# Optimization experiments

Measured on AMD Instinct MI355X. Metric: run time of the kernel, lower is better.

Reference implementation:

```python
import jax, jax.numpy as jnp
import numpy as np

B, L = 128, 256
VOCAB, E, PF = 50000, 300, 50
C, K, R = 512, 3, 53
D3 = (E + 2 * PF) * 3  # 1200, conv input channels


def setup_inputs() -> dict:
    key = jax.random.key(0)
    ks = jax.random.split(key, 12)
    return {
        "context": jax.random.randint(ks[0], (B, L), 0, VOCAB),
        "subject_idx": jnp.sort(jax.random.randint(ks[1], (B, 2), 0, L), axis=-1),
        "object_idx": jnp.sort(jax.random.randint(ks[2], (B, 2), 0, L), axis=-1),
        "subject_dis": jax.random.randint(ks[3], (B, L), 0, 2 * L),
        "object_dis": jax.random.randint(ks[4], (B, L), 0, 2 * L),
        "embed_table": jax.random.normal(ks[5], (VOCAB, E), dtype=jnp.float32),
        "pos_table": jax.random.normal(ks[6], (2 * L, PF), dtype=jnp.float32),
        "conv_w": jax.random.normal(ks[7], (C, D3, K), dtype=jnp.float32) * (1.0 / np.sqrt(D3 * K)),
        "conv_b": jax.random.normal(ks[8], (C,), dtype=jnp.float32) * 0.01,
        "rela_linear_w": jax.random.normal(ks[9], (R, C), dtype=jnp.float32) * (1.0 / np.sqrt(C)),
        "rela_emb": jax.random.normal(ks[10], (R, C), dtype=jnp.float32),
    }


def _span_mean(wf3, idx):
    # mean of wf3[b, start:end+1, :] per sample, vectorized with a mask
    pos = jnp.arange(wf3.shape[1])[None, :]
    m = ((pos >= idx[:, 0:1]) & (pos <= idx[:, 1:2])).astype(wf3.dtype)  # B,L
    return jnp.einsum("bld,bl->bd", wf3, m) / jnp.sum(m, axis=1, keepdims=True)


def reference(context, subject_idx, object_idx, subject_dis, object_dis,
              embed_table, pos_table, conv_w, conv_b, rela_linear_w, rela_emb):
    emb = embed_table[context]                                            # B,L,E
    posf = jnp.concatenate([pos_table[subject_dis], pos_table[object_dis]], axis=2)
    wf = jnp.concatenate([emb, posf], axis=2)                             # B,L,D
    wp = jnp.pad(wf, ((0, 0), (1, 1), (0, 0)))
    # sliding window concat of [i-1, i, i+1]
    wf3 = jnp.concatenate([wp[:, :-2], wp[:, 1:-1], wp[:, 2:]], axis=2)   # B,L,3D

    subj = _span_mean(wf3, subject_idx)                                   # B,3D
    obj = _span_mean(wf3, object_idx)
    rs = jax.nn.softmax(jnp.einsum("bld,bd->bl", wf3, subj), axis=1)
    ro = jax.nn.softmax(jnp.einsum("bld,bd->bl", wf3, obj), axis=1)
    wf3 = wf3 * ((rs + ro) * 0.5)[:, :, None]

    x = jnp.transpose(wf3, (0, 2, 1))                                     # B,3D,L
    y = jax.lax.conv_general_dilated(x, conv_w, (1,), [(K // 2, K // 2)],
                                     dimension_numbers=("NCH", "OIH", "NCH"))
    sent = jnp.transpose(jnp.tanh(y + conv_b[None, :, None]), (0, 2, 1))  # B,L,C

    attn = jnp.einsum("blr,rc->blc",
                      jnp.einsum("blc,rc->blr", sent, rela_linear_w), rela_emb)
    attn = jax.nn.softmax(attn, axis=1)  # softmax over sequence positions
    wo = jnp.max(sent * attn, axis=1)                                     # B,C
    wo = wo / jnp.maximum(jnp.linalg.norm(wo, axis=1, keepdims=True), 1e-12)
    all_dist = jnp.linalg.norm(wo[:, None, :] - rela_emb[None, :, :], axis=2)  # B,R
    return all_dist
```

## Files before the change

### kernel.cpp

```cpp
#include <hip/hip_runtime.h>
#include <hip/hip_bf16.h>
#include <math.h>

#define B_  128
#define L_  256
#define E_  300
#define PF_ 50
#define D_  400
#define D3_ 1200
#define C_  512
#define KW_ 3
#define R_  53
#define M_  (B_*L_)
#define KP_ 1216
#define K3_ (3*KP_)
#define LROWS_ 258

typedef __attribute__((ext_vector_type(8))) short bf16x8;
typedef __attribute__((ext_vector_type(8))) unsigned short u16x8;
typedef __attribute__((ext_vector_type(4))) float f32x4;

__device__ __forceinline__ unsigned short f2bf(float f) {
    union { float f; unsigned u; } x; x.f = f;
    unsigned r = x.u + 0x7FFF + ((x.u >> 16) & 1);
    return (unsigned short)(r >> 16);
}
__device__ __forceinline__ float bf2f(unsigned short u) {
    union { unsigned u; float f; } x; x.u = ((unsigned)u) << 16;
    return x.f;
}

__device__ __forceinline__ void gld16(const void* g, void* l) {
    __builtin_amdgcn_global_load_lds(
        (const __attribute__((address_space(1))) void*)g,
        (__attribute__((address_space(3))) void*)l, 16, 0, 0);
}

__global__ void prep_wpT_kernel(const float* __restrict__ conv_w, unsigned short* __restrict__ WpT) {
    int idx = blockIdx.x * blockDim.x + threadIdx.x;
    if (idx >= C_ * K3_) return;
    int c = idx / K3_, q = idx % K3_;
    int k = q / KP_, ch = q % KP_;
    WpT[idx] = (ch < D3_) ? f2bf(conv_w[c * (D3_ * KW_) + ch * KW_ + k]) : (unsigned short)0;
}

__global__ void prep_mT_kernel(const float* __restrict__ rlw, const float* __restrict__ re,
                               unsigned short* __restrict__ MmatT) {
    int idx = blockIdx.x * blockDim.x + threadIdx.x;
    if (idx >= C_ * C_) return;
    int n = idx / C_, k = idx % C_;
    float acc = 0.f;
    for (int r = 0; r < R_; ++r)
        acc += rlw[r * C_ + k] * re[r * C_ + n];
    MmatT[idx] = f2bf(acc);
}

__global__ void build_wf_kernel(const int* __restrict__ ctx, const int* __restrict__ sdis,
                                const int* __restrict__ odis, const float* __restrict__ emb,
                                const float* __restrict__ pos, float* __restrict__ wf) {
    const int total = M_ * D_;
    for (int idx = blockIdx.x * blockDim.x + threadIdx.x; idx < total;
         idx += gridDim.x * blockDim.x) {
        int d = idx % D_;
        int bt = idx / D_;
        float v;
        if (d < E_)            v = emb[(long)ctx[bt] * E_ + d];
        else if (d < E_ + PF_) v = pos[sdis[bt] * PF_ + (d - E_)];
        else                   v = pos[odis[bt] * PF_ + (d - E_ - PF_)];
        wf[idx] = v;
    }
}

__global__ __launch_bounds__(512) void span_sum_kernel(
    const float* __restrict__ wf, const int* __restrict__ sidx, const int* __restrict__ oidx,
    float* __restrict__ SS, float* __restrict__ OS) {
    const int b = blockIdx.x, e = blockIdx.y;
    const int* idx = e ? oidx : sidx;
    float* out = e ? OS : SS;
    const int s0 = idx[b * 2], s1 = idx[b * 2 + 1];
    const float inv = 1.f / (float)(s1 - s0 + 1);
    const int d = threadIdx.x;
    if (d >= D_) return;

    const float* base_p = wf + (size_t)(b << 8) * D_ + d;
    float base = 0.f;
    for (int t = s0; t <= s1; ++t) base += base_p[(size_t)t * D_];

    float w_s0 = base_p[(size_t)s0 * D_];
    float w_s1 = base_p[(size_t)s1 * D_];
    float j0 = base - w_s1 + ((s0 > 0) ? base_p[(size_t)(s0 - 1) * D_] : 0.f);
    float j2 = base - w_s0 + ((s1 < L_ - 1) ? base_p[(size_t)(s1 + 1) * D_] : 0.f);

    out[((size_t)(b * 3 + 0)) * D_ + d] = j0 * inv;
    out[((size_t)(b * 3 + 1)) * D_ + d] = base * inv;
    out[((size_t)(b * 3 + 2)) * D_ + d] = j2 * inv;
}

__global__ __launch_bounds__(256) void dots_kernel(
    const float* __restrict__ wf, const float* __restrict__ SS, const float* __restrict__ OS,
    float* __restrict__ dsb, float* __restrict__ ddb) {
    const int wave = threadIdx.x >> 6, lane = threadIdx.x & 63;
    const int g = blockIdx.x * 4 + wave;
    const int b = g >> 8, t = g & 255;
    float ds = 0.f, dd = 0.f;
#pragma unroll
    for (int j = 0; j < 3; ++j) {
        int u = t + j - 1;
        if ((unsigned)u < (unsigned)L_) {
            const float4* w  = (const float4*)(wf + ((size_t)((b << 8) + u)) * D_);
            const float4* ss = (const float4*)(SS + ((size_t)(b * 3 + j)) * D_);
            const float4* oo = (const float4*)(OS + ((size_t)(b * 3 + j)) * D_);
            for (int q = lane; q < D_ / 4; q += 64) {
                float4 wv = w[q], sv = ss[q], ov = oo[q];
                ds += wv.x * sv.x + wv.y * sv.y + wv.z * sv.z + wv.w * sv.w;
                dd += wv.x * ov.x + wv.y * ov.y + wv.z * ov.z + wv.w * ov.w;
            }
        }
    }
#pragma unroll
    for (int off = 32; off > 0; off >>= 1) {
        ds += __shfl_down(ds, off);
        dd += __shfl_down(dd, off);
    }
    if (lane == 0) { dsb[g] = ds; ddb[g] = dd; }
}

__global__ __launch_bounds__(256) void softmax_s_kernel(
    const float* __restrict__ dsb, const float* __restrict__ ddb, float* __restrict__ s) {
    const int b = blockIdx.x, tid = threadIdx.x;
    __shared__ float red[256];
    float ds = dsb[(b << 8) + tid];
    float dd = ddb[(b << 8) + tid];

    red[tid] = ds; __syncthreads();
    for (int st = 128; st > 0; st >>= 1) {
        if (tid < st) red[tid] = fmaxf(red[tid], red[tid + st]);
        __syncthreads();
    }
    float ms = red[0]; __syncthreads();
    float es = expf(ds - ms);
    red[tid] = es; __syncthreads();
    for (int st = 128; st > 0; st >>= 1) {
        if (tid < st) red[tid] += red[tid + st];
        __syncthreads();
    }
    float zs = red[0]; __syncthreads();

    red[tid] = dd; __syncthreads();
    for (int st = 128; st > 0; st >>= 1) {
        if (tid < st) red[tid] = fmaxf(red[tid], red[tid + st]);
        __syncthreads();
    }
    float mo = red[0]; __syncthreads();
    float eo = expf(dd - mo);
    red[tid] = eo; __syncthreads();
    for (int st = 128; st > 0; st >>= 1) {
        if (tid < st) red[tid] += red[tid + st];
        __syncthreads();
    }
    float zo = red[0];

    s[(b << 8) + tid] = 0.5f * (es / zs + eo / zo);
}

__global__ void build_xsp_kernel(const float* __restrict__ wf, const float* __restrict__ s,
                                 unsigned short* __restrict__ XSp) {
    const int CH8 = KP_ / 8;
    int idx = blockIdx.x * blockDim.x + threadIdx.x;
    const int total = B_ * LROWS_ * CH8;
    if (idx >= total) return;
    int chunk = idx % CH8;
    int rb = idx / CH8;
    int row = rb % LROWS_;
    int b = rb / LROWS_;

    u16x8 out = {0,0,0,0,0,0,0,0};
    int t = row - 1;
    int ch0 = chunk * 8;
    if ((unsigned)t < (unsigned)L_ && ch0 < D3_) {
        int j = ch0 / D_;
        int d0 = ch0 - j * D_;
        int u = t + j - 1;
        if ((unsigned)u < (unsigned)L_) {
            float sc = s[(b << 8) + t];
            const float* w = wf + ((size_t)((b << 8) + u)) * D_ + d0;
#pragma unroll
            for (int q = 0; q < 8; ++q) out[q] = f2bf(sc * w[q]);
        }
    }
    *(u16x8*)&XSp[((size_t)(b * LROWS_ + row)) * KP_ + ch0] = out;
}

template<int MODE>
__global__ __launch_bounds__(512, 2) void gemm8_kernel(
    const unsigned short* __restrict__ Aglob, const unsigned short* __restrict__ Bglob,
    const float* __restrict__ conv_b, unsigned short* __restrict__ outb,
    float* __restrict__ outf) {
    extern __shared__ unsigned short lds[];
    const int tid = threadIdx.x;
    const int lane = tid & 63;
    const int wave = tid >> 6;
    const int wr = wave >> 2;
    const int wc = wave & 3;
    const int bx = blockIdx.x;
    const int blockN = blockIdx.y * 256;
    const int l15 = lane & 15;
    const int NT = (MODE == 0) ? (K3_ / 64) : (C_ / 64);
    const size_t Astr = (MODE == 0) ? (size_t)KP_ : (size_t)C_;
    const size_t Bstr = (MODE == 0) ? (size_t)K3_ : (size_t)C_;

    const int arole = wc;
    const int bhalf = wc >> 1;
    const int brole = wr * 2 + (wc & 1);

    const int acol0 = (((lane >> 4) + 0) ^ (l15 & 7)) * 8;
    const int acol1 = (((lane >> 4) + 4) ^ (l15 & 7)) * 8;
    const int bro = (wc & 1) * 64;

    auto stageA = [&](int kt, int buf) {
        const unsigned short* gb;
        if constexpr (MODE == 0) {
            int tap = kt / KP_, ch0 = kt - tap * KP_;
            gb = Aglob + ((size_t)(bx * LROWS_ + wr * 128 + tap)) * KP_ + ch0;
        } else {
            gb = Aglob + ((size_t)(bx * 256 + wr * 128)) * C_ + kt;
        }
        unsigned short* pb = &lds[(buf * 2 + wr) * 8192];
#pragma unroll
        for (int i = 0; i < 4; ++i) {
            int sl = arole * 256 + i * 64 + lane;
            int row = sl >> 3, p = sl & 7;
            int colg = p ^ (row & 7);
            gld16(gb + (size_t)row * Astr + colg * 8, (char*)pb + sl * 16);
        }
    };
    auto stageB = [&](int kt, int buf) {
        const unsigned short* gb = Bglob + ((size_t)(blockN + bhalf * 128)) * Bstr + kt;
        unsigned short* pb = &lds[32768 + (buf * 2 + bhalf) * 8192];
#pragma unroll
        for (int i = 0; i < 4; ++i) {
            int sl = brole * 256 + i * 64 + lane;
            int row = sl >> 3, p = sl & 7;
            int colg = p ^ (row & 7);
            gld16(gb + (size_t)row * Bstr + colg * 8, (char*)pb + sl * 16);
        }
    };

    f32x4 acc[8][4] = {};

    stageA(0, 0);
    stageB(0, 0);
    __syncthreads();

    int cur = 0;
    for (int kt = 0; kt < NT * 64; kt += 64, cur ^= 1) {
        int ktn = kt + 64;
        if (ktn >= NT * 64) ktn = 0;
        const unsigned short* Ap = &lds[(cur * 2 + wr) * 8192];
        const unsigned short* Bp = &lds[32768 + (cur * 2 + bhalf) * 8192];

        bf16x8 a[8], b0, b1;

#pragma unroll
        for (int mi = 0; mi < 8; ++mi) a[mi] = *(const bf16x8*)&Ap[(mi * 16 + l15) * 64 + acol0];
        b0 = *(const bf16x8*)&Bp[(bro + 0 * 16 + l15) * 64 + acol0];
        b1 = *(const bf16x8*)&Bp[(bro + 1 * 16 + l15) * 64 + acol0];
        stageA(ktn, cur ^ 1);
        __builtin_amdgcn_s_setprio(1);
#pragma unroll
        for (int mi = 0; mi < 8; ++mi) {
            acc[mi][0] = __builtin_amdgcn_mfma_f32_16x16x32_bf16(a[mi], b0, acc[mi][0], 0, 0, 0);
            acc[mi][1] = __builtin_amdgcn_mfma_f32_16x16x32_bf16(a[mi], b1, acc[mi][1], 0, 0, 0);
        }
        __builtin_amdgcn_s_setprio(0);

        b0 = *(const bf16x8*)&Bp[(bro + 2 * 16 + l15) * 64 + acol0];
        b1 = *(const bf16x8*)&Bp[(bro + 3 * 16 + l15) * 64 + acol0];
        stageB(ktn, cur ^ 1);
        __builtin_amdgcn_s_setprio(1);
#pragma unroll
        for (int mi = 0; mi < 8; ++mi) {
            acc[mi][2] = __builtin_amdgcn_mfma_f32_16x16x32_bf16(a[mi], b0, acc[mi][2], 0, 0, 0);
            acc[mi][3] = __builtin_amdgcn_mfma_f32_16x16x32_bf16(a[mi], b1, acc[mi][3], 0, 0, 0);
        }
        __builtin_amdgcn_s_setprio(0);

#pragma unroll
        for (int mi = 0; mi < 8; ++mi) a[mi] = *(const bf16x8*)&Ap[(mi * 16 + l15) * 64 + acol1];
        b0 = *(const bf16x8*)&Bp[(bro + 0 * 16 + l15) * 64 + acol1];
        b1 = *(const bf16x8*)&Bp[(bro + 1 * 16 + l15) * 64 + acol1];
        __builtin_amdgcn_s_setprio(1);
#pragma unroll
        for (int mi = 0; mi < 8; ++mi) {
            acc[mi][0] = __builtin_amdgcn_mfma_f32_16x16x32_bf16(a[mi], b0, acc[mi][0], 0, 0, 0);
            acc[mi][1] = __builtin_amdgcn_mfma_f32_16x16x32_bf16(a[mi], b1, acc[mi][1], 0, 0, 0);
        }
        __builtin_amdgcn_s_setprio(0);

        b0 = *(const bf16x8*)&Bp[(bro + 2 * 16 + l15) * 64 + acol1];
        b1 = *(const bf16x8*)&Bp[(bro + 3 * 16 + l15) * 64 + acol1];
        __builtin_amdgcn_s_setprio(1);
#pragma unroll
        for (int mi = 0; mi < 8; ++mi) {
            acc[mi][2] = __builtin_amdgcn_mfma_f32_16x16x32_bf16(a[mi], b0, acc[mi][2], 0, 0, 0);
            acc[mi][3] = __builtin_amdgcn_mfma_f32_16x16x32_bf16(a[mi], b1, acc[mi][3], 0, 0, 0);
        }
        __builtin_amdgcn_s_setprio(0);

        __syncthreads();
    }

    const int r4 = ((lane >> 4) << 2);
#pragma unroll
    for (int mi = 0; mi < 8; ++mi) {
#pragma unroll
        for (int nj = 0; nj < 4; ++nj) {
            const int col = blockN + wc * 64 + nj * 16 + l15;
            const int row0 = bx * 256 + wr * 128 + mi * 16 + r4;
            if constexpr (MODE == 0) {
                float bias = conv_b[col];
#pragma unroll
                for (int r = 0; r < 4; ++r)
                    outb[(size_t)(row0 + r) * C_ + col] = f2bf(tanhf(acc[mi][nj][r] + bias));
            } else {
#pragma unroll
                for (int r = 0; r < 4; ++r)
                    outf[(size_t)(row0 + r) * C_ + col] = acc[mi][nj][r];
            }
        }
    }
}

__global__ __launch_bounds__(256) void softmax_wo_kernel(
    const float* __restrict__ P, const unsigned short* __restrict__ sent,
    float* __restrict__ wo) {
    const int b = blockIdx.x;
    const int c = blockIdx.y * 256 + threadIdx.x;
    const float* Pb = P + ((size_t)(b << 8)) * C_ + c;
    const unsigned short* Sb = sent + ((size_t)(b << 8)) * C_ + c;
    float m = -INFINITY;
    for (int l = 0; l < L_; ++l) m = fmaxf(m, Pb[(size_t)l * C_]);
    float z = 0.f, wmax = -INFINITY;
    for (int l = 0; l < L_; ++l) {
        float e = expf(Pb[(size_t)l * C_] - m);
        z += e;
        wmax = fmaxf(wmax, bf2f(Sb[(size_t)l * C_]) * e);
    }
    wo[b * C_ + c] = wmax / z;
}

__global__ __launch_bounds__(256) void final_kernel(
    const float* __restrict__ wo, const float* __restrict__ re, float* __restrict__ out) {
    const int b = blockIdx.x, tid = threadIdx.x;
    __shared__ float won[C_];
    __shared__ float red[256];
    float p = 0.f;
    for (int c = tid; c < C_; c += 256) {
        float v = wo[b * C_ + c];
        p += v * v;
    }
    red[tid] = p; __syncthreads();
    for (int st = 128; st > 0; st >>= 1) {
        if (tid < st) red[tid] += red[tid + st];
        __syncthreads();
    }
    float inv = 1.f / fmaxf(sqrtf(red[0]), 1e-12f);
    for (int c = tid; c < C_; c += 256) won[c] = wo[b * C_ + c] * inv;
    __syncthreads();
    const int wv = tid >> 6, lane = tid & 63;
    for (int r = wv; r < R_; r += 4) {
        float acc2 = 0.f;
        for (int c = lane; c < C_; c += 64) {
            float dlt = won[c] - re[r * C_ + c];
            acc2 += dlt * dlt;
        }
        for (int off = 32; off > 0; off >>= 1) acc2 += __shfl_down(acc2, off);
        if (lane == 0) out[b * R_ + r] = sqrtf(acc2);
    }
}

extern "C" void kernel_launch(void* const* d_in, const int* in_sizes, int n_in,
                              void* d_out, int out_size, void* d_ws, size_t ws_size,
                              hipStream_t stream) {
    const int* context     = (const int*)d_in[0];
    const int* subject_idx = (const int*)d_in[1];
    const int* object_idx  = (const int*)d_in[2];
    const int* subject_dis = (const int*)d_in[3];
    const int* object_dis  = (const int*)d_in[4];
    const float* embed_table = (const float*)d_in[5];
    const float* pos_table   = (const float*)d_in[6];
    const float* conv_w      = (const float*)d_in[7];
    const float* conv_b      = (const float*)d_in[8];
    const float* rlw         = (const float*)d_in[9];
    const float* re          = (const float*)d_in[10];
    float* out = (float*)d_out;

    char* ws = (char*)d_ws;
    size_t off = 0;
    auto alloc = [&](size_t bytes) {
        void* p = ws + off;
        off = (off + bytes + 255) & ~(size_t)255;
        return p;
    };
    float* wf            = (float*)alloc((size_t)M_ * D_ * 4);
    float* s             = (float*)alloc((size_t)M_ * 4);
    unsigned short* XSp  = (unsigned short*)alloc((size_t)B_ * LROWS_ * KP_ * 2);
    unsigned short* WpT  = (unsigned short*)alloc((size_t)C_ * K3_ * 2);
    unsigned short* MmatT= (unsigned short*)alloc((size_t)C_ * C_ * 2);
    unsigned short* sent = (unsigned short*)alloc((size_t)M_ * C_ * 2);
    float* wo            = (float*)alloc((size_t)B_ * C_ * 4);
    float* SS            = (float*)alloc((size_t)B_ * 3 * D_ * 4);
    float* OS            = (float*)alloc((size_t)B_ * 3 * D_ * 4);
    float* dsb           = (float*)alloc((size_t)M_ * 4);
    float* ddb           = (float*)alloc((size_t)M_ * 4);
    float* P = (float*)XSp;

    (void)hipFuncSetAttribute((const void*)gemm8_kernel<0>,
                              hipFuncAttributeMaxDynamicSharedMemorySize, 131072);
    (void)hipFuncSetAttribute((const void*)gemm8_kernel<1>,
                              hipFuncAttributeMaxDynamicSharedMemorySize, 131072);

    prep_wpT_kernel<<<(C_ * K3_ + 255) / 256, 256, 0, stream>>>(conv_w, WpT);
    prep_mT_kernel<<<(C_ * C_ + 255) / 256, 256, 0, stream>>>(rlw, re, MmatT);
    build_wf_kernel<<<4096, 256, 0, stream>>>(context, subject_dis, object_dis,
                                              embed_table, pos_table, wf);
    span_sum_kernel<<<dim3(B_, 2), 512, 0, stream>>>(wf, subject_idx, object_idx, SS, OS);
    dots_kernel<<<M_ / 4, 256, 0, stream>>>(wf, SS, OS, dsb, ddb);
    softmax_s_kernel<<<B_, 256, 0, stream>>>(dsb, ddb, s);
    build_xsp_kernel<<<(B_ * LROWS_ * (KP_ / 8) + 255) / 256, 256, 0, stream>>>(wf, s, XSp);
    gemm8_kernel<0><<<dim3(M_ / 256, C_ / 256), 512, 131072, stream>>>(
        XSp, WpT, conv_b, sent, nullptr);
    gemm8_kernel<1><<<dim3(M_ / 256, C_ / 256), 512, 131072, stream>>>(
        sent, MmatT, nullptr, nullptr, P);
    softmax_wo_kernel<<<dim3(B_, 2), 256, 0, stream>>>(P, sent, wo);
    final_kernel<<<B_, 256, 0, stream>>>(wo, re, out);
}
```

Baseline: 345.6 us.

## Split conv GEMM into quadrant-staged pipeline with interleaved half-tile loads

Replaces the templated conv GEMM with a dedicated kernel that splits the 256x256 block tile into four 128x128 quadrants. Each half-tile of A and B is staged into LDS separately and interleaved with the MFMA work on other quadrants, using explicit vmcnt waits and barriers. This aims to overlap global-to-LDS loads with compute at a finer grain and to shorten the stall before each k-step. The second GEMM becomes a plain specialized kernel with the same logic as before. The hand-tuned waitcnt accounting carries a correctness risk if the outstanding-load counts are wrong.

```diff
diff --git a/kernel.cpp b/kernel.cpp
--- a/kernel.cpp
+++ b/kernel.cpp
@@ -191,11 +191,173 @@
     *(u16x8*)&XSp[((size_t)(b * LROWS_ + row)) * KP_ + ch0] = out;
 }
 
-template<int MODE>
-__global__ __launch_bounds__(512, 2) void gemm8_kernel(
-    const unsigned short* __restrict__ Aglob, const unsigned short* __restrict__ Bglob,
-    const float* __restrict__ conv_b, unsigned short* __restrict__ outb,
-    float* __restrict__ outf) {
+__global__ __launch_bounds__(512, 2) void conv_m201_kernel(
+    const unsigned short* __restrict__ XSp, const unsigned short* __restrict__ WpT,
+    const float* __restrict__ conv_b, unsigned short* __restrict__ sent) {
+    extern __shared__ unsigned short lds[];
+    const int tid = threadIdx.x;
+    const int lane = tid & 63;
+    const int wave = tid >> 6;
+    const int wr2 = wave >> 2;
+    const int wc2 = wave & 3;
+    const int bx = blockIdx.x;
+    const int blockN = blockIdx.y * 256;
+    const int l15 = lane & 15;
+    const int rg = lane >> 4;
+    const int sw = l15 & 7;
+    const int NT = K3_ / 64;
+    const int colk0 = ((0 * 4 + rg) ^ sw) * 8;
+    const int colk1 = ((1 * 4 + rg) ^ sw) * 8;
+
+    auto stageA = [&](int kt, int d, int h) {
+        int tap = kt / KP_, ch0 = kt - tap * KP_;
+        const unsigned short* ga = XSp + ((size_t)(bx * LROWS_ + h * 128 + tap)) * KP_ + ch0;
+        unsigned short* pb = &lds[(d * 2 + h) * 8192];
+#pragma unroll
+        for (int i = 0; i < 2; ++i) {
+            int sl = i * 512 + tid;
+            int row = sl >> 3, p = sl & 7;
+            int colg = p ^ (row & 7);
+            gld16(ga + (size_t)row * KP_ + colg * 8, (char*)pb + sl * 16);
+        }
+    };
+    auto stageB = [&](int kt, int d, int h) {
+        const unsigned short* gb = WpT + ((size_t)(blockN + h * 128)) * K3_ + kt;
+        unsigned short* pb = &lds[32768 + (d * 2 + h) * 8192];
+#pragma unroll
+        for (int i = 0; i < 2; ++i) {
+            int sl = i * 512 + tid;
+            int row = sl >> 3, p = sl & 7;
+            int colg = p ^ (row & 7);
+            gld16(gb + (size_t)row * K3_ + colg * 8, (char*)pb + sl * 16);
+        }
+    };
+
+    f32x4 acc[4][4][2] = {};
+
+    stageA(0, 0, 0); stageB(0, 0, 0); stageA(0, 0, 1); stageB(0, 0, 1);
+    stageA(64 < NT * 64 ? 64 : 0, 1, 0); stageB(64 < NT * 64 ? 64 : 0, 1, 0);
+    asm volatile("s_waitcnt vmcnt(4)" ::: "memory");
+    __builtin_amdgcn_s_barrier();
+
+    int d = 0;
+    for (int t = 0; t < NT; ++t, d ^= 1) {
+        const int t1 = (t + 1 < NT) ? t + 1 : 0;
+        const int t2 = (t + 2 < NT) ? t + 2 : t + 2 - NT;
+        const int kt1 = t1 * 64, kt2 = t2 * 64;
+        const unsigned short* A0 = &lds[(d * 2 + 0) * 8192];
+        const unsigned short* A1 = &lds[(d * 2 + 1) * 8192];
+        const unsigned short* B0 = &lds[32768 + (d * 2 + 0) * 8192];
+        const unsigned short* B1 = &lds[32768 + (d * 2 + 1) * 8192];
+
+        bf16x8 a[4][2], bh0[2][2], bh1[2][2];
+
+#pragma unroll
+        for (int mi = 0; mi < 4; ++mi) {
+            int row = wr2 * 64 + mi * 16 + l15;
+            a[mi][0] = *(const bf16x8*)&A0[row * 64 + colk0];
+            a[mi][1] = *(const bf16x8*)&A0[row * 64 + colk1];
+        }
+#pragma unroll
+        for (int ni = 0; ni < 2; ++ni) {
+            int row = wc2 * 32 + ni * 16 + l15;
+            bh0[ni][0] = *(const bf16x8*)&B0[row * 64 + colk0];
+            bh0[ni][1] = *(const bf16x8*)&B0[row * 64 + colk1];
+        }
+        stageB(kt1, d ^ 1, 1);
+        __builtin_amdgcn_s_barrier();
+        __builtin_amdgcn_s_setprio(1);
+#pragma unroll
+        for (int mi = 0; mi < 4; ++mi)
+#pragma unroll
+            for (int ni = 0; ni < 2; ++ni)
+#pragma unroll
+                for (int ks = 0; ks < 2; ++ks)
+                    acc[0][mi][ni] = __builtin_amdgcn_mfma_f32_16x16x32_bf16(
+                        a[mi][ks], bh0[ni][ks], acc[0][mi][ni], 0, 0, 0);
+        __builtin_amdgcn_s_setprio(0);
+        __builtin_amdgcn_s_barrier();
+
+#pragma unroll
+        for (int ni = 0; ni < 2; ++ni) {
+            int row = wc2 * 32 + ni * 16 + l15;
+            bh1[ni][0] = *(const bf16x8*)&B1[row * 64 + colk0];
+            bh1[ni][1] = *(const bf16x8*)&B1[row * 64 + colk1];
+        }
+        stageA(kt1, d ^ 1, 1);
+        asm volatile("s_waitcnt vmcnt(6)" ::: "memory");
+        __builtin_amdgcn_s_barrier();
+        __builtin_amdgcn_s_setprio(1);
+#pragma unroll
+        for (int mi = 0; mi < 4; ++mi)
+#pragma unroll
+            for (int ni = 0; ni < 2; ++ni)
+#pragma unroll
+                for (int ks = 0; ks < 2; ++ks)
+                    acc[1][mi][ni] = __builtin_amdgcn_mfma_f32_16x16x32_bf16(
+                        a[mi][ks], bh1[ni][ks], acc[1][mi][ni], 0, 0, 0);
+        __builtin_amdgcn_s_setprio(0);
+        __builtin_amdgcn_s_barrier();
+
+#pragma unroll
+        for (int mi = 0; mi < 4; ++mi) {
+            int row = wr2 * 64 + mi * 16 + l15;
+            a[mi][0] = *(const bf16x8*)&A1[row * 64 + colk0];
+            a[mi][1] = *(const bf16x8*)&A1[row * 64 + colk1];
+        }
+        stageA(kt2, d, 0);
+        __builtin_amdgcn_s_barrier();
+        __builtin_amdgcn_s_setprio(1);
+#pragma unroll
+        for (int mi = 0; mi < 4; ++mi)
+#pragma unroll
+            for (int ni = 0; ni < 2; ++ni)
+#pragma unroll
+                for (int ks = 0; ks < 2; ++ks)
+                    acc[2][mi][ni] = __builtin_amdgcn_mfma_f32_16x16x32_bf16(
+                        a[mi][ks], bh0[ni][ks], acc[2][mi][ni], 0, 0, 0);
+        __builtin_amdgcn_s_setprio(0);
+        __builtin_amdgcn_s_barrier();
+
+        stageB(kt2, d, 0);
+        asm volatile("s_waitcnt vmcnt(6)" ::: "memory");
+        __builtin_amdgcn_s_barrier();
+        __builtin_amdgcn_s_setprio(1);
+#pragma unroll
+        for (int mi = 0; mi < 4; ++mi)
+#pragma unroll
+            for (int ni = 0; ni < 2; ++ni)
+#pragma unroll
+                for (int ks = 0; ks < 2; ++ks)
+                    acc[3][mi][ni] = __builtin_amdgcn_mfma_f32_16x16x32_bf16(
+                        a[mi][ks], bh1[ni][ks], acc[3][mi][ni], 0, 0, 0);
+        __builtin_amdgcn_s_setprio(0);
+        __builtin_amdgcn_s_barrier();
+    }
+
+    asm volatile("s_waitcnt vmcnt(0)" ::: "memory");
+
+    const int r4 = (lane >> 4) << 2;
+#pragma unroll
+    for (int q = 0; q < 4; ++q) {
+#pragma unroll
+        for (int mi = 0; mi < 4; ++mi) {
+#pragma unroll
+            for (int ni = 0; ni < 2; ++ni) {
+                const int col = blockN + (q & 1) * 128 + wc2 * 32 + ni * 16 + l15;
+                const int row0 = bx * 256 + (q >> 1) * 128 + wr2 * 64 + mi * 16 + r4;
+                float bias = conv_b[col];
+#pragma unroll
+                for (int r = 0; r < 4; ++r)
+                    sent[(size_t)(row0 + r) * C_ + col] = f2bf(tanhf(acc[q][mi][ni][r] + bias));
+            }
+        }
+    }
+}
+
+__global__ __launch_bounds__(512, 2) void pgemm_kernel(
+    const unsigned short* __restrict__ sent, const unsigned short* __restrict__ MmatT,
+    float* __restrict__ P) {
     extern __shared__ unsigned short lds[];
     const int tid = threadIdx.x;
     const int lane = tid & 63;
@@ -205,9 +367,7 @@
     const int bx = blockIdx.x;
     const int blockN = blockIdx.y * 256;
     const int l15 = lane & 15;
-    const int NT = (MODE == 0) ? (K3_ / 64) : (C_ / 64);
-    const size_t Astr = (MODE == 0) ? (size_t)KP_ : (size_t)C_;
-    const size_t Bstr = (MODE == 0) ? (size_t)K3_ : (size_t)C_;
+    const int NT = C_ / 64;
 
     const int arole = wc;
     const int bhalf = wc >> 1;
@@ -218,31 +378,25 @@
     const int bro = (wc & 1) * 64;
 
     auto stageA = [&](int kt, int buf) {
-        const unsigned short* gb;
-        if constexpr (MODE == 0) {
-            int tap = kt / KP_, ch0 = kt - tap * KP_;
-            gb = Aglob + ((size_t)(bx * LROWS_ + wr * 128 + tap)) * KP_ + ch0;
-        } else {
-            gb = Aglob + ((size_t)(bx * 256 + wr * 128)) * C_ + kt;
-        }
+        const unsigned short* gb = sent + ((size_t)(bx * 256 + wr * 128)) * C_ + kt;
         unsigned short* pb = &lds[(buf * 2 + wr) * 8192];
 #pragma unroll
         for (int i = 0; i < 4; ++i) {
             int sl = arole * 256 + i * 64 + lane;
             int row = sl >> 3, p = sl & 7;
             int colg = p ^ (row & 7);
-            gld16(gb + (size_t)row * Astr + colg * 8, (char*)pb + sl * 16);
+            gld16(gb + (size_t)row * C_ + colg * 8, (char*)pb + sl * 16);
         }
     };
     auto stageB = [&](int kt, int buf) {
-        const unsigned short* gb = Bglob + ((size_t)(blockN + bhalf * 128)) * Bstr + kt;
+        const unsigned short* gb = MmatT + ((size_t)(blockN + bhalf * 128)) * C_ + kt;
         unsigned short* pb = &lds[32768 + (buf * 2 + bhalf) * 8192];
 #pragma unroll
         for (int i = 0; i < 4; ++i) {
             int sl = brole * 256 + i * 64 + lane;
             int row = sl >> 3, p = sl & 7;
             int colg = p ^ (row & 7);
-            gld16(gb + (size_t)row * Bstr + colg * 8, (char*)pb + sl * 16);
+            gld16(gb + (size_t)row * C_ + colg * 8, (char*)pb + sl * 16);
         }
     };
 
@@ -317,16 +471,9 @@
         for (int nj = 0; nj < 4; ++nj) {
             const int col = blockN + wc * 64 + nj * 16 + l15;
             const int row0 = bx * 256 + wr * 128 + mi * 16 + r4;
-            if constexpr (MODE == 0) {
-                float bias = conv_b[col];
-#pragma unroll
-                for (int r = 0; r < 4; ++r)
-                    outb[(size_t)(row0 + r) * C_ + col] = f2bf(tanhf(acc[mi][nj][r] + bias));
-            } else {
-#pragma unroll
-                for (int r = 0; r < 4; ++r)
-                    outf[(size_t)(row0 + r) * C_ + col] = acc[mi][nj][r];
-            }
+#pragma unroll
+            for (int r = 0; r < 4; ++r)
+                P[(size_t)(row0 + r) * C_ + col] = acc[mi][nj][r];
         }
     }
 }
@@ -415,9 +562,9 @@
     float* ddb           = (float*)alloc((size_t)M_ * 4);
     float* P = (float*)XSp;
 
-    (void)hipFuncSetAttribute((const void*)gemm8_kernel<0>,
+    (void)hipFuncSetAttribute((const void*)conv_m201_kernel,
                               hipFuncAttributeMaxDynamicSharedMemorySize, 131072);
-    (void)hipFuncSetAttribute((const void*)gemm8_kernel<1>,
+    (void)hipFuncSetAttribute((const void*)pgemm_kernel,
                               hipFuncAttributeMaxDynamicSharedMemorySize, 131072);
 
     prep_wpT_kernel<<<(C_ * K3_ + 255) / 256, 256, 0, stream>>>(conv_w, WpT);
@@ -428,10 +575,9 @@
     dots_kernel<<<M_ / 4, 256, 0, stream>>>(wf, SS, OS, dsb, ddb);
     softmax_s_kernel<<<B_, 256, 0, stream>>>(dsb, ddb, s);
     build_xsp_kernel<<<(B_ * LROWS_ * (KP_ / 8) + 255) / 256, 256, 0, stream>>>(wf, s, XSp);
-    gemm8_kernel<0><<<dim3(M_ / 256, C_ / 256), 512, 131072, stream>>>(
-        XSp, WpT, conv_b, sent, nullptr);
-    gemm8_kernel<1><<<dim3(M_ / 256, C_ / 256), 512, 131072, stream>>>(
-        sent, MmatT, nullptr, nullptr, P);
+    conv_m201_kernel<<<dim3(M_ / 256, C_ / 256), 512, 131072, stream>>>(
+        XSp, WpT, conv_b, sent);
+    pgemm_kernel<<<dim3(M_ / 256, C_ / 256), 512, 131072, stream>>>(sent, MmatT, P);
     softmax_wo_kernel<<<dim3(B_, 2), 256, 0, stream>>>(P, sent, wo);
     final_kernel<<<B_, 256, 0, stream>>>(wo, re, out);
 }
```

Result: slower. 356.1 us (+3.0%).

## Split conv GEMM into dedicated kernel with triple-buffered 32-wide K pipeline

Applied to the files above, without the earlier changes.

The conv GEMM gets its own kernel. It uses a K tile of 32 instead of 64 and triple-buffered LDS with two tiles in flight, waiting on a partial vmcnt before each barrier so loads overlap the MFMAs. The LDS swizzle changes to a rotation pattern suited to 32-element rows, and dynamic LDS drops to 96KB. This should hide more global load latency, at the cost of twice as many barriers and loop iterations per K. The second GEMM is moved unchanged into a specialised non-templated kernel.

```diff
diff --git a/kernel.cpp b/kernel.cpp
--- a/kernel.cpp
+++ b/kernel.cpp
@@ -191,11 +191,9 @@
     *(u16x8*)&XSp[((size_t)(b * LROWS_ + row)) * KP_ + ch0] = out;
 }
 
-template<int MODE>
-__global__ __launch_bounds__(512, 2) void gemm8_kernel(
-    const unsigned short* __restrict__ Aglob, const unsigned short* __restrict__ Bglob,
-    const float* __restrict__ conv_b, unsigned short* __restrict__ outb,
-    float* __restrict__ outf) {
+__global__ __launch_bounds__(512, 2) void conv32_kernel(
+    const unsigned short* __restrict__ XSp, const unsigned short* __restrict__ WpT,
+    const float* __restrict__ conv_b, unsigned short* __restrict__ sent) {
     extern __shared__ unsigned short lds[];
     const int tid = threadIdx.x;
     const int lane = tid & 63;
@@ -205,44 +203,140 @@
     const int bx = blockIdx.x;
     const int blockN = blockIdx.y * 256;
     const int l15 = lane & 15;
-    const int NT = (MODE == 0) ? (K3_ / 64) : (C_ / 64);
-    const size_t Astr = (MODE == 0) ? (size_t)KP_ : (size_t)C_;
-    const size_t Bstr = (MODE == 0) ? (size_t)K3_ : (size_t)C_;
-
+    const int NT = K3_ / 32;
     const int arole = wc;
     const int bhalf = wc >> 1;
     const int brole = wr * 2 + (wc & 1);
+    const int bro = (wc & 1) * 64;
+    const int acolp = (((lane >> 4) + (l15 >> 1)) & 3) * 8;
+
+    auto stageA = [&](int kt, int buf) {
+        int tap = kt / KP_, ch0 = kt - tap * KP_;
+        const unsigned short* ga = XSp + ((size_t)(bx * LROWS_ + wr * 128 + tap)) * KP_ + ch0;
+        unsigned short* pb = &lds[(buf * 2 + wr) * 4096];
+#pragma unroll
+        for (int i = 0; i < 2; ++i) {
+            int sl = arole * 128 + i * 64 + lane;
+            int row = sl >> 2, p = sl & 3;
+            int g = (p - (row >> 1)) & 3;
+            gld16(ga + (size_t)row * KP_ + g * 8, (char*)pb + sl * 16);
+        }
+    };
+    auto stageB = [&](int kt, int buf) {
+        const unsigned short* gb = WpT + ((size_t)(blockN + bhalf * 128)) * K3_ + kt;
+        unsigned short* pb = &lds[16384 + (buf * 2 + bhalf) * 4096];
+#pragma unroll
+        for (int i = 0; i < 2; ++i) {
+            int sl = brole * 128 + i * 64 + lane;
+            int row = sl >> 2, p = sl & 3;
+            int g = (p - (row >> 1)) & 3;
+            gld16(gb + (size_t)row * K3_ + g * 8, (char*)pb + sl * 16);
+        }
+    };
+
+    f32x4 acc[8][4] = {};
+
+    stageA(0, 0); stageB(0, 0);
+    stageA(32, 1); stageB(32, 1);
+    asm volatile("s_waitcnt vmcnt(4)" ::: "memory");
+    __builtin_amdgcn_s_barrier();
+    asm volatile("" ::: "memory");
+
+    int cur = 0, tgt = 2;
+    for (int t = 0; t < NT; ++t) {
+        int t2 = t + 2;
+        if (t2 >= NT) t2 -= NT;
+        const int kt2 = t2 * 32;
+        const unsigned short* Ap = &lds[(cur * 2 + wr) * 4096];
+        const unsigned short* Bp = &lds[16384 + (cur * 2 + bhalf) * 4096];
+
+        bf16x8 a[8], b[4];
+#pragma unroll
+        for (int mi = 0; mi < 8; ++mi)
+            a[mi] = *(const bf16x8*)&Ap[(mi * 16 + l15) * 32 + acolp];
+#pragma unroll
+        for (int ni = 0; ni < 4; ++ni)
+            b[ni] = *(const bf16x8*)&Bp[(bro + ni * 16 + l15) * 32 + acolp];
+
+        stageA(kt2, tgt);
+        stageB(kt2, tgt);
+
+        __builtin_amdgcn_s_setprio(1);
+#pragma unroll
+        for (int mi = 0; mi < 8; ++mi)
+#pragma unroll
+            for (int ni = 0; ni < 4; ++ni)
+                acc[mi][ni] = __builtin_amdgcn_mfma_f32_16x16x32_bf16(
+                    a[mi], b[ni], acc[mi][ni], 0, 0, 0);
+        __builtin_amdgcn_s_setprio(0);
+
+        asm volatile("s_waitcnt vmcnt(4)" ::: "memory");
+        __builtin_amdgcn_s_barrier();
+        asm volatile("" ::: "memory");
+
+        cur = (cur == 2) ? 0 : cur + 1;
+        tgt = (tgt == 2) ? 0 : tgt + 1;
+    }
+
+    asm volatile("s_waitcnt vmcnt(0)" ::: "memory");
+
+    const int r4 = ((lane >> 4) << 2);
+#pragma unroll
+    for (int mi = 0; mi < 8; ++mi) {
+#pragma unroll
+        for (int nj = 0; nj < 4; ++nj) {
+            const int col = blockN + wc * 64 + nj * 16 + l15;
+            const int row0 = bx * 256 + wr * 128 + mi * 16 + r4;
+            float bias = conv_b[col];
+#pragma unroll
+            for (int r = 0; r < 4; ++r)
+                sent[(size_t)(row0 + r) * C_ + col] = f2bf(tanhf(acc[mi][nj][r] + bias));
+        }
+    }
+}
+
+__global__ __launch_bounds__(512, 2) void pgemm_kernel(
+    const unsigned short* __restrict__ sent, const unsigned short* __restrict__ MmatT,
+    float* __restrict__ P) {
+    extern __shared__ unsigned short lds[];
+    const int tid = threadIdx.x;
+    const int lane = tid & 63;
+    const int wave = tid >> 6;
+    const int wr = wave >> 2;
+    const int wc = wave & 3;
+    const int bx = blockIdx.x;
+    const int blockN = blockIdx.y * 256;
+    const int l15 = lane & 15;
+    const int NT = C_ / 64;
+
+    const int arole = wc;
+    const int bhalf = wc >> 1;
+    const int brole = wr * 2 + (wc & 1);
 
     const int acol0 = (((lane >> 4) + 0) ^ (l15 & 7)) * 8;
     const int acol1 = (((lane >> 4) + 4) ^ (l15 & 7)) * 8;
     const int bro = (wc & 1) * 64;
 
     auto stageA = [&](int kt, int buf) {
-        const unsigned short* gb;
-        if constexpr (MODE == 0) {
-            int tap = kt / KP_, ch0 = kt - tap * KP_;
-            gb = Aglob + ((size_t)(bx * LROWS_ + wr * 128 + tap)) * KP_ + ch0;
-        } else {
-            gb = Aglob + ((size_t)(bx * 256 + wr * 128)) * C_ + kt;
-        }
+        const unsigned short* gb = sent + ((size_t)(bx * 256 + wr * 128)) * C_ + kt;
         unsigned short* pb = &lds[(buf * 2 + wr) * 8192];
 #pragma unroll
         for (int i = 0; i < 4; ++i) {
             int sl = arole * 256 + i * 64 + lane;
             int row = sl >> 3, p = sl & 7;
             int colg = p ^ (row & 7);
-            gld16(gb + (size_t)row * Astr + colg * 8, (char*)pb + sl * 16);
+            gld16(gb + (size_t)row * C_ + colg * 8, (char*)pb + sl * 16);
         }
     };
     auto stageB = [&](int kt, int buf) {
-        const unsigned short* gb = Bglob + ((size_t)(blockN + bhalf * 128)) * Bstr + kt;
+        const unsigned short* gb = MmatT + ((size_t)(blockN + bhalf * 128)) * C_ + kt;
         unsigned short* pb = &lds[32768 + (buf * 2 + bhalf) * 8192];
 #pragma unroll
         for (int i = 0; i < 4; ++i) {
             int sl = brole * 256 + i * 64 + lane;
             int row = sl >> 3, p = sl & 7;
             int colg = p ^ (row & 7);
-            gld16(gb + (size_t)row * Bstr + colg * 8, (char*)pb + sl * 16);
+            gld16(gb + (size_t)row * C_ + colg * 8, (char*)pb + sl * 16);
         }
     };
 
@@ -317,16 +411,9 @@
         for (int nj = 0; nj < 4; ++nj) {
             const int col = blockN + wc * 64 + nj * 16 + l15;
             const int row0 = bx * 256 + wr * 128 + mi * 16 + r4;
-            if constexpr (MODE == 0) {
-                float bias = conv_b[col];
-#pragma unroll
-                for (int r = 0; r < 4; ++r)
-                    outb[(size_t)(row0 + r) * C_ + col] = f2bf(tanhf(acc[mi][nj][r] + bias));
-            } else {
-#pragma unroll
-                for (int r = 0; r < 4; ++r)
-                    outf[(size_t)(row0 + r) * C_ + col] = acc[mi][nj][r];
-            }
+#pragma unroll
+            for (int r = 0; r < 4; ++r)
+                P[(size_t)(row0 + r) * C_ + col] = acc[mi][nj][r];
         }
     }
 }
@@ -415,9 +502,9 @@
     float* ddb           = (float*)alloc((size_t)M_ * 4);
     float* P = (float*)XSp;
 
-    (void)hipFuncSetAttribute((const void*)gemm8_kernel<0>,
-                              hipFuncAttributeMaxDynamicSharedMemorySize, 131072);
-    (void)hipFuncSetAttribute((const void*)gemm8_kernel<1>,
+    (void)hipFuncSetAttribute((const void*)conv32_kernel,
+                              hipFuncAttributeMaxDynamicSharedMemorySize, 98304);
+    (void)hipFuncSetAttribute((const void*)pgemm_kernel,
                               hipFuncAttributeMaxDynamicSharedMemorySize, 131072);
 
     prep_wpT_kernel<<<(C_ * K3_ + 255) / 256, 256, 0, stream>>>(conv_w, WpT);
@@ -428,10 +515,9 @@
     dots_kernel<<<M_ / 4, 256, 0, stream>>>(wf, SS, OS, dsb, ddb);
     softmax_s_kernel<<<B_, 256, 0, stream>>>(dsb, ddb, s);
     build_xsp_kernel<<<(B_ * LROWS_ * (KP_ / 8) + 255) / 256, 256, 0, stream>>>(wf, s, XSp);
-    gemm8_kernel<0><<<dim3(M_ / 256, C_ / 256), 512, 131072, stream>>>(
-        XSp, WpT, conv_b, sent, nullptr);
-    gemm8_kernel<1><<<dim3(M_ / 256, C_ / 256), 512, 131072, stream>>>(
-        sent, MmatT, nullptr, nullptr, P);
+    conv32_kernel<<<dim3(M_ / 256, C_ / 256), 512, 98304, stream>>>(
+        XSp, WpT, conv_b, sent);
+    pgemm_kernel<<<dim3(M_ / 256, C_ / 256), 512, 131072, stream>>>(sent, MmatT, P);
     softmax_wo_kernel<<<dim3(B_, 2), 256, 0, stream>>>(P, sent, wo);
     final_kernel<<<B_, 256, 0, stream>>>(wo, re, out);
 }
```

Result: slower. 360.4 us (+4.3%).
